# Kernel tuning notes

Hardware: AMD Instinct MI355X
Metric: run time of the kernel (lower is better)

The kernel has to match this reference:

```python
import jax, jax.numpy as jnp
import numpy as np

EPS = 1e-5

def _neighbor_idx(H, W):
    # flat index of the 3x3 clamped neighborhood for each pixel, [H*W, 9]
    r = np.arange(H)[:, None, None]  # [H,1,1]
    c = np.arange(W)[None, :, None]  # [1,W,1]
    dr = np.repeat(np.array([-1, 0, 1]), 3)[None, None, :]  # [1,1,9]
    dc = np.tile(np.array([-1, 0, 1]), 3)[None, None, :]
    ri = np.clip(r + dr, 0, H - 1)
    ci = np.clip(c + dc, 0, W - 1)
    return jnp.asarray((ri * W + ci).reshape(H * W, 9))

def setup_inputs() -> dict:
    key = jax.random.key(0)
    ks = jax.random.split(key, 7)
    B, C, H, W = 16, 256, 80, 80
    s = 1.0 / np.sqrt(C)
    return {
        "x": jax.random.normal(ks[0], (B, C, H, W), jnp.float32),
        "Wq": jax.random.normal(ks[1], (C, C), jnp.float32) * s,
        "bq": jax.random.normal(ks[2], (C,), jnp.float32) * s,
        "Wk": jax.random.normal(ks[3], (C, C), jnp.float32) * s,
        "bk": jax.random.normal(ks[4], (C,), jnp.float32) * s,
        "Wv": jax.random.normal(ks[5], (C, C), jnp.float32) * s,
        "bv": jax.random.normal(ks[6], (C,), jnp.float32) * s,
    }

def reference(x, Wq, bq, Wk, bk, Wv, bv):
    B, C, H, W = x.shape
    N = H * W
    xf = x.reshape(B, C, N)
    # 1x1 convs as channel GEMMs
    q = jnp.einsum('oc,bcn->bno', Wq, xf) + bq          # [B,N,C]
    k = jnp.einsum('oc,bcn->bon', Wk, xf) + bk[:, None]  # [B,C,N]
    v = jnp.einsum('oc,bcn->bon', Wv, xf) + bv[:, None]  # [B,C,N]
    idx = _neighbor_idx(H, W)                            # [N,9]
    k_n = k[:, :, idx]                                   # [B,C,N,9]
    v_n = v[:, :, idx]                                   # [B,C,N,9]
    # raw attention scores (NOT softmaxed before AV, matching the source)
    scores = jnp.einsum('bnc,bcnq->bnq', q, k_n)         # [B,N,9]
    new_v = jnp.einsum('bnq,bcnq->bcn', scores, v_n).reshape(B, C, H, W)
    out9 = scores.reshape(B, H, W, 9)
    center = out9[..., 4]
    others_mean = (out9.sum(-1) - center) / 8.0
    output = jnp.stack([center, others_mean], axis=-1)   # [B,H,W,2]
    # residual + layer_norm over [H,W] (no affine), per (B,C)
    xr = x + new_v
    mu = xr.mean(axis=(-2, -1), keepdims=True)
    var = ((xr - mu) ** 2).mean(axis=(-2, -1), keepdims=True)
    x_out = (xr - mu) * jax.lax.rsqrt(var + EPS)
    return (output, x_out)
```

## Files before the change

kernel.cpp:

```cpp
#include <hip/hip_runtime.h>
#include <hip/hip_bf16.h>

using f32x4  = __attribute__((ext_vector_type(4))) float;
using short8 = __attribute__((ext_vector_type(8))) short;
using bf16   = __hip_bfloat16;

constexpr int BATCH = 16;
constexpr int CH    = 256;
constexpr int HH    = 80;
constexpr int WW    = 80;
constexpr int NPIX  = HH * WW;

__device__ __forceinline__ float b2f(unsigned short u) {
    union { unsigned int i; float f; } x;
    x.i = ((unsigned int)u) << 16;
    return x.f;
}

typedef __attribute__((address_space(3))) void  lds_void;
typedef __attribute__((address_space(1))) const void glb_void;
__device__ __forceinline__ void glds16(const void* g, void* l) {
    __builtin_amdgcn_global_load_lds((glb_void*)(unsigned long long)g,
                                     (lds_void*)(unsigned int)(unsigned long long)l,
                                     16, 0, 0);
}

__global__ __launch_bounds__(256) void convert_w(
    const float* __restrict__ Wq, const float* __restrict__ Wk,
    const float* __restrict__ Wv, bf16* __restrict__ Wb)
{
    const int elem = blockIdx.x * 256 + threadIdx.x;
    const int mat  = blockIdx.y;
    const float* src = (mat == 0) ? Wq : (mat == 1) ? Wk : Wv;
    Wb[(size_t)mat * CH * CH + elem] = __float2bfloat16(src[elem]);
}

__global__ __launch_bounds__(256) void transpose_cast(
    const float* __restrict__ x, bf16* __restrict__ xt, int b0)
{
    __shared__ float t[64][65];
    const int b  = b0 + blockIdx.z;
    const int n0 = blockIdx.x * 64;
    const int c0 = blockIdx.y * 64;
    const float* xb = x + (size_t)b * CH * NPIX;
    const int tid = threadIdx.x;

    {
        const int nl  = tid & 63;
        const int cl0 = tid >> 6;
        #pragma unroll
        for (int i = 0; i < 16; ++i) {
            const int cl = cl0 + i * 4;
            t[cl][nl] = xb[(size_t)(c0 + cl) * NPIX + n0 + nl];
        }
    }
    __syncthreads();
    {
        bf16* xtb = xt + (size_t)blockIdx.z * NPIX * CH;
        const int cl  = tid & 63;
        const int nl0 = tid >> 6;
        #pragma unroll
        for (int i = 0; i < 16; ++i) {
            const int nl = nl0 + i * 4;
            xtb[(size_t)(n0 + nl) * CH + c0 + cl] = __float2bfloat16(t[cl][nl]);
        }
    }
}

__global__ __launch_bounds__(256, 2) void qkv_mfma(
    const bf16* __restrict__ xt, const bf16* __restrict__ Wb,
    const float* __restrict__ bq, const float* __restrict__ bk,
    const float* __restrict__ bv,
    bf16* __restrict__ qo, bf16* __restrict__ ko, bf16* __restrict__ vt)
{
    const int m  = blockIdx.z % 3;
    const int bl = blockIdx.z / 3;
    const int n0 = blockIdx.x * 128;
    const int o0 = blockIdx.y * 128;
    const bf16*  W    = Wb + (size_t)m * CH * CH;
    const float* bias = (m == 0) ? bq : (m == 1) ? bk : bv;
    const bf16*  A    = xt + (size_t)bl * NPIX * CH;

    __shared__ char As[2][128 * 64];
    __shared__ char Bs[2][128 * 64];

    const int tid = threadIdx.x;
    const int wv  = tid >> 6, ln = tid & 63;
    const int wr  = wv >> 1,  wc = wv & 1;
    const int lm  = ln & 15,  lk = ln >> 4;

    f32x4 acc[4][4];
    #pragma unroll
    for (int i = 0; i < 4; ++i)
        #pragma unroll
        for (int j = 0; j < 4; ++j)
            #pragma unroll
            for (int r = 0; r < 4; ++r) acc[i][j][r] = 0.f;

    auto stage = [&](int buf, int k0) {
        #pragma unroll
        for (int it = 0; it < 2; ++it) {
            const int idx = it * 256 + tid;
            const int row = idx >> 2;
            const int pos = idx & 3;
            const int chk = pos ^ ((row >> 1) & 3);
            glds16(A + (size_t)(n0 + row) * CH + k0 + chk * 8, &As[buf][idx * 16]);
            glds16(W + (size_t)(o0 + row) * CH + k0 + chk * 8, &Bs[buf][idx * 16]);
        }
    };

    stage(0, 0);
    int buf = 0;
    #pragma unroll
    for (int t = 0; t < 8; ++t) {
        __syncthreads();
        if (t < 7) stage(buf ^ 1, (t + 1) * 32);

        short8 afr[4], bfr[4];
        #pragma unroll
        for (int i = 0; i < 4; ++i) {
            const int row = wr * 64 + i * 16 + lm;
            const int chk = lk ^ ((row >> 1) & 3);
            afr[i] = *(const short8*)&As[buf][row * 64 + chk * 16];
        }
        #pragma unroll
        for (int j = 0; j < 4; ++j) {
            const int row = wc * 64 + j * 16 + lm;
            const int chk = lk ^ ((row >> 1) & 3);
            bfr[j] = *(const short8*)&Bs[buf][row * 64 + chk * 16];
        }
        if (m < 2) {
            #pragma unroll
            for (int i = 0; i < 4; ++i)
                #pragma unroll
                for (int j = 0; j < 4; ++j)
                    acc[i][j] = __builtin_amdgcn_mfma_f32_16x16x32_bf16(
                        bfr[j], afr[i], acc[i][j], 0, 0, 0);
        } else {
            #pragma unroll
            for (int i = 0; i < 4; ++i)
                #pragma unroll
                for (int j = 0; j < 4; ++j)
                    acc[i][j] = __builtin_amdgcn_mfma_f32_16x16x32_bf16(
                        afr[i], bfr[j], acc[i][j], 0, 0, 0);
        }
        buf ^= 1;
    }

    if (m < 2) {
        bf16* out = (m == 0 ? qo : ko) + (size_t)bl * NPIX * CH;
        #pragma unroll
        for (int j = 0; j < 4; ++j) {
            const int ob = o0 + wc * 64 + j * 16 + lk * 4;
            const float4 b4 = *(const float4*)(bias + ob);
            #pragma unroll
            for (int i = 0; i < 4; ++i) {
                const int n = n0 + wr * 64 + i * 16 + lm;
                ushort4 pk;
                {
                    const bf16 h0 = __float2bfloat16(acc[i][j][0] + b4.x);
                    const bf16 h1 = __float2bfloat16(acc[i][j][1] + b4.y);
                    const bf16 h2 = __float2bfloat16(acc[i][j][2] + b4.z);
                    const bf16 h3 = __float2bfloat16(acc[i][j][3] + b4.w);
                    pk.x = *(const unsigned short*)&h0;
                    pk.y = *(const unsigned short*)&h1;
                    pk.z = *(const unsigned short*)&h2;
                    pk.w = *(const unsigned short*)&h3;
                }
                *(ushort4*)(out + (size_t)n * CH + ob) = pk;
            }
        }
    } else {
        bf16* out = vt + (size_t)bl * CH * NPIX;
        #pragma unroll
        for (int j = 0; j < 4; ++j) {
            const int o = o0 + wc * 64 + j * 16 + lm;
            const float bs = bias[o];
            #pragma unroll
            for (int i = 0; i < 4; ++i) {
                const int nb = n0 + wr * 64 + i * 16 + lk * 4;
                ushort4 pk;
                #pragma unroll
                for (int r = 0; r < 4; ++r) {
                    const bf16 h = __float2bfloat16(acc[i][j][r] + bs);
                    ((unsigned short*)&pk)[r] = *(const unsigned short*)&h;
                }
                *(ushort4*)(out + (size_t)o * NPIX + nb) = pk;
            }
        }
    }
}

__global__ __launch_bounds__(256) void scores_kernel(
    const bf16* __restrict__ q, const bf16* __restrict__ k,
    float* __restrict__ scores, float* __restrict__ out0, int b0)
{
    const int wave = threadIdx.x >> 6, lane = threadIdx.x & 63;
    const int n  = blockIdx.x * 4 + wave;
    const int bl = blockIdx.y;
    const int b  = b0 + bl;

    const unsigned short* qrow = (const unsigned short*)(q + ((size_t)bl * NPIX + n) * CH) + lane * 4;
    const unsigned short* kb   = (const unsigned short*)(k + (size_t)bl * NPIX * CH);

    const ushort4 qu = *(const ushort4*)qrow;
    const float q0 = b2f(qu.x), q1 = b2f(qu.y), q2 = b2f(qu.z), q3 = b2f(qu.w);

    const int r = n / WW, col = n % WW;
    float s[9], ssum = 0.f;
    #pragma unroll
    for (int j = 0; j < 9; ++j) {
        const int rr = min(max(r + j / 3 - 1, 0), HH - 1);
        const int c2 = min(max(col + j % 3 - 1, 0), WW - 1);
        const int nbr = rr * WW + c2;
        const ushort4 kv = *(const ushort4*)(kb + (size_t)nbr * CH + lane * 4);
        float d = q0 * b2f(kv.x) + q1 * b2f(kv.y) + q2 * b2f(kv.z) + q3 * b2f(kv.w);
        #pragma unroll
        for (int off = 32; off >= 1; off >>= 1) d += __shfl_xor(d, off, 64);
        s[j] = d;
        ssum += d;
    }
    if (lane == 0) {
        float* sp = scores + (size_t)bl * 9 * NPIX;
        #pragma unroll
        for (int j = 0; j < 9; ++j) sp[(size_t)j * NPIX + n] = s[j];
        const float center = s[4];
        out0[((size_t)b * NPIX + n) * 2 + 0] = center;
        out0[((size_t)b * NPIX + n) * 2 + 1] = (ssum - center) * 0.125f;
    }
}

__global__ __launch_bounds__(320) void newv_ln(
    const float* __restrict__ x, const bf16* __restrict__ vt,
    const float* __restrict__ scores, float* __restrict__ xout, int b0)
{
    __shared__ __align__(16) unsigned short lds_v[NPIX];
    __shared__ float rsum[5], rsq[5];

    const int c  = blockIdx.x;
    const int bl = blockIdx.y;
    const int b  = b0 + bl;
    const int tid = threadIdx.x;

    const unsigned short* vrow = (const unsigned short*)(vt + ((size_t)bl * CH + c) * NPIX);
    const float* xrow = x + ((size_t)b * CH + c) * NPIX;
    const float* sb   = scores + (size_t)bl * 9 * NPIX;

    #pragma unroll
    for (int i = 0; i < 3; ++i) {
        const int t = tid + i * 320;
        if (t < NPIX / 8) ((int4*)lds_v)[t] = ((const int4*)vrow)[t];
    }
    __syncthreads();

    float val[20];
    float sum = 0.f, sq = 0.f;
    #pragma unroll
    for (int it = 0; it < 5; ++it) {
        const int p   = tid + it * 320;
        const int n0  = p * 4;
        const int r   = p / 20;
        const int c0  = (p % 20) * 4;

        const int rm = max(r - 1, 0) * WW;
        const int r0 = r * WW;
        const int rp = min(r + 1, HH - 1) * WW;

        float4 s[9];
        #pragma unroll
        for (int j = 0; j < 9; ++j)
            s[j] = *(const float4*)(sb + (size_t)j * NPIX + n0);

        const float4 xin = *(const float4*)(xrow + n0);

        const int cA = max(c0 - 1, 0);
        const int cF = min(c0 + 4, WW - 1);
        float vm[6], v0[6], vp[6];
        vm[0] = b2f(lds_v[rm + cA]); v0[0] = b2f(lds_v[r0 + cA]); vp[0] = b2f(lds_v[rp + cA]);
        #pragma unroll
        for (int t = 1; t < 5; ++t) {
            vm[t] = b2f(lds_v[rm + c0 + t - 1]);
            v0[t] = b2f(lds_v[r0 + c0 + t - 1]);
            vp[t] = b2f(lds_v[rp + c0 + t - 1]);
        }
        vm[5] = b2f(lds_v[rm + cF]); v0[5] = b2f(lds_v[r0 + cF]); vp[5] = b2f(lds_v[rp + cF]);

        #pragma unroll
        for (int px = 0; px < 4; ++px) {
            const float sc0 = ((const float*)&s[0])[px];
            const float sc1 = ((const float*)&s[1])[px];
            const float sc2 = ((const float*)&s[2])[px];
            const float sc3 = ((const float*)&s[3])[px];
            const float sc4 = ((const float*)&s[4])[px];
            const float sc5 = ((const float*)&s[5])[px];
            const float sc6 = ((const float*)&s[6])[px];
            const float sc7 = ((const float*)&s[7])[px];
            const float sc8 = ((const float*)&s[8])[px];
            float a;
            a  = sc0 * vm[px] + sc1 * vm[px + 1] + sc2 * vm[px + 2];
            a += sc3 * v0[px] + sc4 * v0[px + 1] + sc5 * v0[px + 2];
            a += sc6 * vp[px] + sc7 * vp[px + 1] + sc8 * vp[px + 2];
            const float vv = ((const float*)&xin)[px] + a;
            val[it * 4 + px] = vv;
            sum += vv;
            sq  += vv * vv;
        }
    }

    #pragma unroll
    for (int off = 32; off >= 1; off >>= 1) {
        sum += __shfl_xor(sum, off, 64);
        sq  += __shfl_xor(sq,  off, 64);
    }
    const int wave = tid >> 6, lane = tid & 63;
    if (lane == 0) { rsum[wave] = sum; rsq[wave] = sq; }
    __syncthreads();
    sum = rsum[0] + rsum[1] + rsum[2] + rsum[3] + rsum[4];
    sq  = rsq[0]  + rsq[1]  + rsq[2]  + rsq[3]  + rsq[4];

    const float mu   = sum * (1.f / NPIX);
    const float var  = sq * (1.f / NPIX) - mu * mu;
    const float rstd = rsqrtf(var + 1e-5f);

    float* orow = xout + ((size_t)b * CH + c) * NPIX;
    #pragma unroll
    for (int it = 0; it < 5; ++it) {
        const int n0 = (tid + it * 320) * 4;
        float4 o;
        o.x = (val[it * 4 + 0] - mu) * rstd;
        o.y = (val[it * 4 + 1] - mu) * rstd;
        o.z = (val[it * 4 + 2] - mu) * rstd;
        o.w = (val[it * 4 + 3] - mu) * rstd;
        *(float4*)(orow + n0) = o;
    }
}

extern "C" void kernel_launch(void* const* d_in, const int* in_sizes, int n_in,
                              void* d_out, int out_size, void* d_ws, size_t ws_size,
                              hipStream_t stream)
{
    const float* x  = (const float*)d_in[0];
    const float* Wq = (const float*)d_in[1];
    const float* bq = (const float*)d_in[2];
    const float* Wk = (const float*)d_in[3];
    const float* bk = (const float*)d_in[4];
    const float* Wv = (const float*)d_in[5];
    const float* bv = (const float*)d_in[6];

    float* out0 = (float*)d_out;
    float* xout = out0 + (size_t)BATCH * NPIX * 2;

    char* ws = (char*)d_ws;
    bf16* Wb = (bf16*)ws;
    ws += (size_t)3 * CH * CH * sizeof(bf16);

    const size_t fBF = (size_t)NPIX * CH * sizeof(bf16);
    const size_t fSC = (size_t)NPIX * 9 * sizeof(float);
    const size_t perBatch = 4 * fBF + fSC;

    size_t avail = ws_size - ((size_t)3 * CH * CH * sizeof(bf16));
    int NB = (int)(avail / perBatch);
    if (NB < 1)  NB = 1;
    if (NB > BATCH) NB = BATCH;

    bf16*  xt  = (bf16*)ws;
    bf16*  qb  = (bf16*)(ws + (size_t)NB * fBF);
    bf16*  kb  = (bf16*)(ws + (size_t)NB * fBF * 2);
    bf16*  vt  = (bf16*)(ws + (size_t)NB * fBF * 3);
    float* sc  = (float*)(ws + (size_t)NB * fBF * 4);

    convert_w<<<dim3(CH * CH / 256, 3), 256, 0, stream>>>(Wq, Wk, Wv, Wb);

    for (int b0 = 0; b0 < BATCH; b0 += NB) {
        const int cnb = (BATCH - b0 < NB) ? (BATCH - b0) : NB;

        transpose_cast<<<dim3(NPIX / 64, CH / 64, cnb), 256, 0, stream>>>(x, xt, b0);

        qkv_mfma<<<dim3(NPIX / 128, CH / 128, cnb * 3), 256, 0, stream>>>(
            xt, Wb, bq, bk, bv, qb, kb, vt);

        scores_kernel<<<dim3(NPIX / 4, cnb), 256, 0, stream>>>(qb, kb, sc, out0, b0);

        newv_ln<<<dim3(CH, cnb), 320, 0, stream>>>(x, vt, sc, xout, b0);
    }
}
```

Baseline: 281.0 us.

## Fuse Q/K/V projections per block and compute scores from channel-major layout

The QKV GEMM now loads each 128-pixel activation tile into LDS once and reuses it for all three weight matrices, streaming only the weight tiles. Q and K are written channel-major like V. The scores kernel then gives each thread four consecutive pixels, loops over channels, and reuses contiguous K row loads across the 3x3 neighborhood instead of doing per-pixel wave reductions. The transpose kernel is also changed to write four packed bf16 values per store. In exchange, the GEMM uses a large 64KB A tile in LDS, which limits occupancy, and the scores kernel launches far fewer, smaller blocks with a long serial channel loop.

```diff
diff --git a/kernel.cpp b/kernel.cpp
--- a/kernel.cpp
+++ b/kernel.cpp
@@ -57,12 +57,18 @@
     __syncthreads();
     {
         bf16* xtb = xt + (size_t)blockIdx.z * NPIX * CH;
-        const int cl  = tid & 63;
-        const int nl0 = tid >> 6;
-        #pragma unroll
-        for (int i = 0; i < 16; ++i) {
-            const int nl = nl0 + i * 4;
-            xtb[(size_t)(n0 + nl) * CH + c0 + cl] = __float2bfloat16(t[cl][nl]);
+        const int cp  = (tid & 15) * 4;
+        const int nl0 = tid >> 4;
+        #pragma unroll
+        for (int i = 0; i < 4; ++i) {
+            const int nl = nl0 + i * 16;
+            ushort4 pk;
+            #pragma unroll
+            for (int j = 0; j < 4; ++j) {
+                const bf16 h = __float2bfloat16(t[cp + j][nl]);
+                ((unsigned short*)&pk)[j] = *(const unsigned short*)&h;
+            }
+            *(ushort4*)(xtb + (size_t)(n0 + nl) * CH + c0 + cp) = pk;
         }
     }
 }
@@ -71,17 +77,14 @@
     const bf16* __restrict__ xt, const bf16* __restrict__ Wb,
     const float* __restrict__ bq, const float* __restrict__ bk,
     const float* __restrict__ bv,
-    bf16* __restrict__ qo, bf16* __restrict__ ko, bf16* __restrict__ vt)
-{
-    const int m  = blockIdx.z % 3;
-    const int bl = blockIdx.z / 3;
+    bf16* __restrict__ qt, bf16* __restrict__ kt, bf16* __restrict__ vt)
+{
+    const int bl = blockIdx.z;
     const int n0 = blockIdx.x * 128;
     const int o0 = blockIdx.y * 128;
-    const bf16*  W    = Wb + (size_t)m * CH * CH;
-    const float* bias = (m == 0) ? bq : (m == 1) ? bk : bv;
-    const bf16*  A    = xt + (size_t)bl * NPIX * CH;
-
-    __shared__ char As[2][128 * 64];
+    const bf16* A = xt + (size_t)bl * NPIX * CH;
+
+    __shared__ char As[128 * 512];
     __shared__ char Bs[2][128 * 64];
 
     const int tid = threadIdx.x;
@@ -89,89 +92,75 @@
     const int wr  = wv >> 1,  wc = wv & 1;
     const int lm  = ln & 15,  lk = ln >> 4;
 
-    f32x4 acc[4][4];
-    #pragma unroll
-    for (int i = 0; i < 4; ++i)
-        #pragma unroll
-        for (int j = 0; j < 4; ++j)
-            #pragma unroll
-            for (int r = 0; r < 4; ++r) acc[i][j][r] = 0.f;
-
-    auto stage = [&](int buf, int k0) {
+    #pragma unroll
+    for (int t = 0; t < 16; ++t) {
+        const int idx = t * 256 + tid;
+        const int row = idx >> 5, pos = idx & 31;
+        const int chk = pos ^ (row & 7);
+        glds16(A + (size_t)(n0 + row) * CH + chk * 8, &As[idx * 16]);
+    }
+
+    auto stageB = [&](int buf, const bf16* Wm, int k0) {
         #pragma unroll
         for (int it = 0; it < 2; ++it) {
             const int idx = it * 256 + tid;
-            const int row = idx >> 2;
-            const int pos = idx & 3;
+            const int row = idx >> 2, pos = idx & 3;
             const int chk = pos ^ ((row >> 1) & 3);
-            glds16(A + (size_t)(n0 + row) * CH + k0 + chk * 8, &As[buf][idx * 16]);
-            glds16(W + (size_t)(o0 + row) * CH + k0 + chk * 8, &Bs[buf][idx * 16]);
+            glds16(Wm + (size_t)(o0 + row) * CH + k0 + chk * 8, &Bs[buf][idx * 16]);
         }
     };
 
-    stage(0, 0);
+    stageB(0, Wb, 0);
     int buf = 0;
-    #pragma unroll
-    for (int t = 0; t < 8; ++t) {
-        __syncthreads();
-        if (t < 7) stage(buf ^ 1, (t + 1) * 32);
-
-        short8 afr[4], bfr[4];
-        #pragma unroll
-        for (int i = 0; i < 4; ++i) {
-            const int row = wr * 64 + i * 16 + lm;
-            const int chk = lk ^ ((row >> 1) & 3);
-            afr[i] = *(const short8*)&As[buf][row * 64 + chk * 16];
-        }
-        #pragma unroll
-        for (int j = 0; j < 4; ++j) {
-            const int row = wc * 64 + j * 16 + lm;
-            const int chk = lk ^ ((row >> 1) & 3);
-            bfr[j] = *(const short8*)&Bs[buf][row * 64 + chk * 16];
-        }
-        if (m < 2) {
-            #pragma unroll
-            for (int i = 0; i < 4; ++i)
+
+    bf16* const outs[3] = { qt + (size_t)bl * CH * NPIX,
+                            kt + (size_t)bl * CH * NPIX,
+                            vt + (size_t)bl * CH * NPIX };
+    const float* const biases[3] = { bq, bk, bv };
+
+    #pragma unroll
+    for (int m = 0; m < 3; ++m) {
+        f32x4 acc[4][4];
+        #pragma unroll
+        for (int i = 0; i < 4; ++i)
+            #pragma unroll
+            for (int j = 0; j < 4; ++j)
                 #pragma unroll
-                for (int j = 0; j < 4; ++j)
-                    acc[i][j] = __builtin_amdgcn_mfma_f32_16x16x32_bf16(
-                        bfr[j], afr[i], acc[i][j], 0, 0, 0);
-        } else {
+                for (int r = 0; r < 4; ++r) acc[i][j][r] = 0.f;
+
+        #pragma unroll
+        for (int t = 0; t < 8; ++t) {
+            __syncthreads();
+            const int s = m * 8 + t;
+            if (s < 23) {
+                const int ns = s + 1;
+                stageB(buf ^ 1, Wb + (size_t)(ns >> 3) * CH * CH, (ns & 7) * 32);
+            }
+
+            short8 afr[4], bfr[4];
+            #pragma unroll
+            for (int i = 0; i < 4; ++i) {
+                const int row = wr * 64 + i * 16 + lm;
+                const int chunk = (t * 4 + lk) ^ (row & 7);
+                afr[i] = *(const short8*)&As[row * 512 + chunk * 16];
+            }
+            #pragma unroll
+            for (int j = 0; j < 4; ++j) {
+                const int row = wc * 64 + j * 16 + lm;
+                const int chk = lk ^ ((row >> 1) & 3);
+                bfr[j] = *(const short8*)&Bs[buf][row * 64 + chk * 16];
+            }
             #pragma unroll
             for (int i = 0; i < 4; ++i)
                 #pragma unroll
                 for (int j = 0; j < 4; ++j)
                     acc[i][j] = __builtin_amdgcn_mfma_f32_16x16x32_bf16(
                         afr[i], bfr[j], acc[i][j], 0, 0, 0);
-        }
-        buf ^= 1;
-    }
-
-    if (m < 2) {
-        bf16* out = (m == 0 ? qo : ko) + (size_t)bl * NPIX * CH;
-        #pragma unroll
-        for (int j = 0; j < 4; ++j) {
-            const int ob = o0 + wc * 64 + j * 16 + lk * 4;
-            const float4 b4 = *(const float4*)(bias + ob);
-            #pragma unroll
-            for (int i = 0; i < 4; ++i) {
-                const int n = n0 + wr * 64 + i * 16 + lm;
-                ushort4 pk;
-                {
-                    const bf16 h0 = __float2bfloat16(acc[i][j][0] + b4.x);
-                    const bf16 h1 = __float2bfloat16(acc[i][j][1] + b4.y);
-                    const bf16 h2 = __float2bfloat16(acc[i][j][2] + b4.z);
-                    const bf16 h3 = __float2bfloat16(acc[i][j][3] + b4.w);
-                    pk.x = *(const unsigned short*)&h0;
-                    pk.y = *(const unsigned short*)&h1;
-                    pk.z = *(const unsigned short*)&h2;
-                    pk.w = *(const unsigned short*)&h3;
-                }
-                *(ushort4*)(out + (size_t)n * CH + ob) = pk;
-            }
-        }
-    } else {
-        bf16* out = vt + (size_t)bl * CH * NPIX;
+            buf ^= 1;
+        }
+
+        bf16* out = outs[m];
+        const float* bias = biases[m];
         #pragma unroll
         for (int j = 0; j < 4; ++j) {
             const int o = o0 + wc * 64 + j * 16 + lm;
@@ -191,43 +180,86 @@
     }
 }
 
-__global__ __launch_bounds__(256) void scores_kernel(
-    const bf16* __restrict__ q, const bf16* __restrict__ k,
+__global__ __launch_bounds__(64) void scores_kernel(
+    const bf16* __restrict__ qt, const bf16* __restrict__ kt,
     float* __restrict__ scores, float* __restrict__ out0, int b0)
 {
-    const int wave = threadIdx.x >> 6, lane = threadIdx.x & 63;
-    const int n  = blockIdx.x * 4 + wave;
+    const int qi = blockIdx.x * 64 + threadIdx.x;
     const int bl = blockIdx.y;
     const int b  = b0 + bl;
-
-    const unsigned short* qrow = (const unsigned short*)(q + ((size_t)bl * NPIX + n) * CH) + lane * 4;
-    const unsigned short* kb   = (const unsigned short*)(k + (size_t)bl * NPIX * CH);
-
-    const ushort4 qu = *(const ushort4*)qrow;
-    const float q0 = b2f(qu.x), q1 = b2f(qu.y), q2 = b2f(qu.z), q3 = b2f(qu.w);
-
-    const int r = n / WW, col = n % WW;
-    float s[9], ssum = 0.f;
+    const int n0 = qi * 4;
+    const int r  = qi / 20;
+    const int p0 = n0 - r * WW;
+
+    const unsigned short* qp = (const unsigned short*)(qt + (size_t)bl * NPIX * CH);
+    const unsigned short* kp = (const unsigned short*)(kt + (size_t)bl * NPIX * CH);
+
+    const int rbm = max(r - 1, 0) * WW;
+    const int rb0 = r * WW;
+    const int rbp = min(r + 1, HH - 1) * WW;
+    const bool eL = (p0 == 0), eR = (p0 == 76);
+
+    float acc[4][9];
+    #pragma unroll
+    for (int px = 0; px < 4; ++px)
+        #pragma unroll
+        for (int j = 0; j < 9; ++j) acc[px][j] = 0.f;
+
+    #pragma unroll 2
+    for (int c = 0; c < CH; ++c) {
+        const size_t cb = (size_t)c * NPIX;
+        const ushort4 qv = *(const ushort4*)(qp + cb + n0);
+        const float qf0 = b2f(qv.x), qf1 = b2f(qv.y), qf2 = b2f(qv.z), qf3 = b2f(qv.w);
+
+        #pragma unroll
+        for (int dr = 0; dr < 3; ++dr) {
+            const int rb = (dr == 0) ? rbm : (dr == 1) ? rb0 : rbp;
+            const unsigned short* kr = kp + cb + rb + p0;
+            const ushort2 wl = *(const ushort2*)(kr - 2);
+            const ushort4 wm = *(const ushort4*)(kr);
+            const ushort2 wr2 = *(const ushort2*)(kr + 4);
+            const float w3 = b2f(wl.y);
+            const float w4 = b2f(wm.x), w5 = b2f(wm.y), w6 = b2f(wm.z), w7 = b2f(wm.w);
+            const float w8 = b2f(wr2.x);
+
+            acc[0][dr*3+0] += qf0 * w3;
+            acc[0][dr*3+1] += qf0 * w4;
+            acc[0][dr*3+2] += qf0 * w5;
+            acc[1][dr*3+0] += qf1 * w4;
+            acc[1][dr*3+1] += qf1 * w5;
+            acc[1][dr*3+2] += qf1 * w6;
+            acc[2][dr*3+0] += qf2 * w5;
+            acc[2][dr*3+1] += qf2 * w6;
+            acc[2][dr*3+2] += qf2 * w7;
+            acc[3][dr*3+0] += qf3 * w6;
+            acc[3][dr*3+1] += qf3 * w7;
+            acc[3][dr*3+2] += qf3 * w8;
+            if (eL) acc[0][dr*3+0] += qf0 * (w4 - w3);
+            if (eR) acc[3][dr*3+2] += qf3 * (w7 - w8);
+        }
+    }
+
+    float* sp = scores + (size_t)bl * 9 * NPIX;
     #pragma unroll
     for (int j = 0; j < 9; ++j) {
-        const int rr = min(max(r + j / 3 - 1, 0), HH - 1);
-        const int c2 = min(max(col + j % 3 - 1, 0), WW - 1);
-        const int nbr = rr * WW + c2;
-        const ushort4 kv = *(const ushort4*)(kb + (size_t)nbr * CH + lane * 4);
-        float d = q0 * b2f(kv.x) + q1 * b2f(kv.y) + q2 * b2f(kv.z) + q3 * b2f(kv.w);
-        #pragma unroll
-        for (int off = 32; off >= 1; off >>= 1) d += __shfl_xor(d, off, 64);
-        s[j] = d;
-        ssum += d;
-    }
-    if (lane == 0) {
-        float* sp = scores + (size_t)bl * 9 * NPIX;
-        #pragma unroll
-        for (int j = 0; j < 9; ++j) sp[(size_t)j * NPIX + n] = s[j];
-        const float center = s[4];
-        out0[((size_t)b * NPIX + n) * 2 + 0] = center;
-        out0[((size_t)b * NPIX + n) * 2 + 1] = (ssum - center) * 0.125f;
-    }
+        float4 v = { acc[0][j], acc[1][j], acc[2][j], acc[3][j] };
+        *(float4*)(sp + (size_t)j * NPIX + n0) = v;
+    }
+    float ssum[4];
+    #pragma unroll
+    for (int px = 0; px < 4; ++px) {
+        float s = 0.f;
+        #pragma unroll
+        for (int j = 0; j < 9; ++j) s += acc[px][j];
+        ssum[px] = s;
+    }
+    float* op = out0 + ((size_t)b * NPIX + n0) * 2;
+    float4 o0v = { acc[0][4], (ssum[0] - acc[0][4]) * 0.125f,
+                   acc[1][4], (ssum[1] - acc[1][4]) * 0.125f };
+    float4 o1v = { acc[2][4], (ssum[2] - acc[2][4]) * 0.125f,
+                   acc[3][4], (ssum[3] - acc[3][4]) * 0.125f };
+    *(float4*)(op)     = o0v;
+    *(float4*)(op + 4) = o1v;
 }
 
 __global__ __launch_bounds__(320) void newv_ln(
@@ -364,9 +396,9 @@
     if (NB > BATCH) NB = BATCH;
 
     bf16*  xt  = (bf16*)ws;
-    bf16*  qb  = (bf16*)(ws + (size_t)NB * fBF);
-    bf16*  kb  = (bf16*)(ws + (size_t)NB * fBF * 2);
-    bf16*  vt  = (bf16*)(ws + (size_t)NB * fBF * 3);
+    bf16*  qtb = (bf16*)(ws + (size_t)NB * fBF);
+    bf16*  ktb = (bf16*)(ws + (size_t)NB * fBF * 2);
+    bf16*  vtb = (bf16*)(ws + (size_t)NB * fBF * 3);
     float* sc  = (float*)(ws + (size_t)NB * fBF * 4);
 
     convert_w<<<dim3(CH * CH / 256, 3), 256, 0, stream>>>(Wq, Wk, Wv, Wb);
@@ -376,11 +408,11 @@
 
         transpose_cast<<<dim3(NPIX / 64, CH / 64, cnb), 256, 0, stream>>>(x, xt, b0);
 
-        qkv_mfma<<<dim3(NPIX / 128, CH / 128, cnb * 3), 256, 0, stream>>>(
-            xt, Wb, bq, bk, bv, qb, kb, vt);
-
-        scores_kernel<<<dim3(NPIX / 4, cnb), 256, 0, stream>>>(qb, kb, sc, out0, b0);
-
-        newv_ln<<<dim3(CH, cnb), 320, 0, stream>>>(x, vt, sc, xout, b0);
-    }
-}
+        qkv_mfma<<<dim3(NPIX / 128, CH / 128, cnb), 256, 0, stream>>>(
+            xt, Wb, bq, bk, bv, qtb, ktb, vtb);
+
+        scores_kernel<<<dim3(NPIX / 256, cnb), 64, 0, stream>>>(qtb, ktb, sc, out0, b0);
+
+        newv_ln<<<dim3(CH, cnb), 320, 0, stream>>>(x, vtb, sc, xout, b0);
+    }
+}
```

New measurement: 325.4 us. 1.16x slower.
